# Optimization experiments

Measured on AMD Instinct MI355X. Metric: run time of the kernel, lower is better.

## Reference

```python
import jax, jax.numpy as jnp
import numpy as np

N = 100000          # nodes
E = 1600000         # edges
D_IN = 128
HID = 256
N_CLASSES = 10
N_GRAPHS = 64


def gcn_conv(x, src, dst, W, b, n_nodes):
    """PyG GCNConv: add self-loops, symmetric deg^{-1/2} normalization, x@W, scatter-add."""
    h = x @ W  # [N, out]
    loop = jnp.arange(n_nodes, dtype=src.dtype)
    src2 = jnp.concatenate([src, loop])
    dst2 = jnp.concatenate([dst, loop])
    deg = jax.ops.segment_sum(jnp.ones(src2.shape[0], x.dtype), dst2, num_segments=n_nodes)
    dinv = jax.lax.rsqrt(deg)  # deg >= 1 thanks to self-loops
    norm = dinv[src2] * dinv[dst2]  # [E+N]
    msg = norm[:, None] * h[src2]   # [E+N, out]
    return jax.ops.segment_sum(msg, dst2, num_segments=n_nodes) + b


def setup_inputs() -> dict:
    key = jax.random.key(0)
    ks = jax.random.split(key, 12)
    x = jax.random.normal(ks[0], (N, D_IN), dtype=jnp.float32)
    edge_index = jax.random.randint(ks[1], (2, E), 0, N, dtype=jnp.int64)
    batch = jnp.sort(jax.random.randint(ks[2], (N,), 0, N_GRAPHS, dtype=jnp.int64))
    def glorot(k, shape):
        lim = float(np.sqrt(6.0 / (shape[0] + shape[1])))
        return jax.random.uniform(k, shape, jnp.float32, -lim, lim)
    W1 = glorot(ks[3], (D_IN, HID));  b1 = jnp.zeros((HID,), jnp.float32)
    W2 = glorot(ks[4], (HID, HID));   b2 = jnp.zeros((HID,), jnp.float32)
    Wf1 = glorot(ks[5], (HID, HID));  bf1 = jnp.zeros((HID,), jnp.float32)
    Wf2 = glorot(ks[6], (HID, N_CLASSES)); bf2 = jnp.zeros((N_CLASSES,), jnp.float32)
    return {"x": x, "edge_index": edge_index, "batch": batch,
            "W1": W1, "b1": b1, "W2": W2, "b2": b2,
            "Wf1": Wf1, "bf1": bf1, "Wf2": Wf2, "bf2": bf2}


def reference(x, edge_index, batch, W1, b1, W2, b2, Wf1, bf1, Wf2, bf2):
    src, dst = edge_index[0], edge_index[1]
    h = jax.nn.relu(gcn_conv(x, src, dst, W1, b1, N))
    h = jax.nn.relu(gcn_conv(h, src, dst, W2, b2, N))
    # global mean pool over graph ids
    summed = jax.ops.segment_sum(h, batch, num_segments=N_GRAPHS)  # [G, HID]
    counts = jax.ops.segment_sum(jnp.ones((N,), h.dtype), batch, num_segments=N_GRAPHS)
    pooled = summed / jnp.maximum(counts, 1.0)[:, None]
    z = jax.nn.relu(pooled @ Wf1 + bf1)
    alpha = jax.nn.softplus(z @ Wf2 + bf2) + 0.001
    return alpha
```

## Files before the change

kernel.cpp:

```cpp
#include <hip/hip_runtime.h>
#include <math.h>

#define NN   100000
#define NE   1600000
#define DIN  128
#define HID  256
#define NG   64
#define NCLS 10

#define NBLK 128
#define EPB  (NE / NBLK)
#define NBUK 512
#define NPB  196
#define NHIST (NBUK * NBLK)
#define NBR  ((NN + 127) / 128)

using bf16x8 = __attribute__((ext_vector_type(8))) short;
using f32x4  = __attribute__((ext_vector_type(4))) float;
using f32x2  = __attribute__((ext_vector_type(2))) float;
using u32x2  = __attribute__((ext_vector_type(2))) unsigned int;
using u32x4  = __attribute__((ext_vector_type(4))) unsigned int;

static __device__ __forceinline__ unsigned short f2bf(float f) {
    unsigned u = __float_as_uint(f);
    u += 0x7fff + ((u >> 16) & 1);
    return (unsigned short)(u >> 16);
}

static __device__ __forceinline__ unsigned char f32_to_fp8(float f) {
    float a = fminf(fabsf(f), 448.f);
    unsigned bits = __float_as_uint(a * 0x1p-120f);
    bits += 0x7ffff + ((bits >> 20) & 1);
    unsigned e4 = (bits >> 20) & 0x7f;
    return (unsigned char)(e4 | (f < 0.f ? 0x80u : 0u));
}
#if __has_builtin(__builtin_amdgcn_cvt_pk_f32_fp8)
#define HAVE_CVT_FP8 1
#endif
static __device__ __forceinline__ void fp8x4_to_f32(unsigned u, float* f) {
#ifdef HAVE_CVT_FP8
    f32x2 lo = __builtin_amdgcn_cvt_pk_f32_fp8((int)u, false);
    f32x2 hi = __builtin_amdgcn_cvt_pk_f32_fp8((int)u, true);
    f[0] = lo[0]; f[1] = lo[1]; f[2] = hi[0]; f[3] = hi[1];
#else
#pragma unroll
    for (int k = 0; k < 4; ++k) {
        unsigned b = (u >> (8 * k)) & 0xffu;
        unsigned bits = ((b & 0x80u) << 24) | ((b & 0x7fu) << 20);
        f[k] = __uint_as_float(bits) * 0x1p+120f;
    }
#endif
}
static __device__ __forceinline__ int4 fp8x8_to_bf16x8(unsigned lo, unsigned hi) {
    float f[8];
    fp8x4_to_f32(lo, f);
    fp8x4_to_f32(hi, f + 4);
    int4 r;
    r.x = (int)((__float_as_uint(f[0]) >> 16) | (__float_as_uint(f[1]) & 0xffff0000u));
    r.y = (int)((__float_as_uint(f[2]) >> 16) | (__float_as_uint(f[3]) & 0xffff0000u));
    r.z = (int)((__float_as_uint(f[4]) >> 16) | (__float_as_uint(f[5]) & 0xffff0000u));
    r.w = (int)((__float_as_uint(f[6]) >> 16) | (__float_as_uint(f[7]) & 0xffff0000u));
    return r;
}


__global__ __launch_bounds__(256) void k_hist(const int* __restrict__ dst,
                                              int* __restrict__ histg) {
    __shared__ int h[NBUK];
    const int t = threadIdx.x;
    for (int i = t; i < NBUK; i += 256) h[i] = 0;
    __syncthreads();
    const int e0 = blockIdx.x * EPB, e1 = e0 + EPB;
    for (int e = e0 + t; e < e1; e += 256)
        atomicAdd(&h[(unsigned)__builtin_nontemporal_load(&dst[e]) / NPB], 1);
    __syncthreads();
    for (int i = t; i < NBUK; i += 256)
        histg[i * NBLK + blockIdx.x] = h[i];
}

__global__ __launch_bounds__(256) void k_bsum2(const int* __restrict__ d,
                                               int* __restrict__ bsum) {
    __shared__ int sd[256];
    int t = threadIdx.x;
    const int4 v = *(const int4*)&d[blockIdx.x * 1024 + t * 4];
    sd[t] = v.x + v.y + v.z + v.w;
    __syncthreads();
    for (int off = 128; off > 0; off >>= 1) {
        if (t < off) sd[t] += sd[t + off];
        __syncthreads();
    }
    if (t == 0) bsum[blockIdx.x] = sd[0];
}

__global__ void k_scanb2(const int* __restrict__ bsum, int* __restrict__ boff,
                         const int* __restrict__ batch, float* __restrict__ countsf) {
    __shared__ int tmp[64];
    int t = threadIdx.x;
    int v = bsum[t];
    tmp[t] = v; __syncthreads();
    for (int off = 1; off < 64; off <<= 1) {
        int u = (t >= off) ? tmp[t - off] : 0;
        __syncthreads();
        tmp[t] += u;
        __syncthreads();
    }
    boff[t] = tmp[t] - v;
    int g = t;
    int lo = 0, hi = NN;
    while (lo < hi) { int mid = (lo + hi) >> 1; if (batch[mid] < g) lo = mid + 1; else hi = mid; }
    int lb = lo;
    lo = 0; hi = NN;
    while (lo < hi) { int mid = (lo + hi) >> 1; if (batch[mid] <= g) lo = mid + 1; else hi = mid; }
    countsf[g] = (float)(lo - lb);
}

__global__ __launch_bounds__(256) void k_offs2(int* __restrict__ d,
                                               const int* __restrict__ boff) {
    __shared__ int ts[256];
    int t = threadIdx.x;
    int base = blockIdx.x * 1024 + t * 4;
    int4 v = *(const int4*)&d[base];
    int s = v.x + v.y + v.z + v.w;
    ts[t] = s; __syncthreads();
    for (int off = 1; off < 256; off <<= 1) {
        int u = (t >= off) ? ts[t - off] : 0;
        __syncthreads();
        ts[t] += u;
        __syncthreads();
    }
    int run = ts[t] - s + boff[blockIdx.x];
    int4 o;
    o.x = run; run += v.x;
    o.y = run; run += v.y;
    o.z = run; run += v.z;
    o.w = run; run += v.w;
    *(int4*)&d[base] = o;
}

__global__ __launch_bounds__(256) void k_scatter(const int* __restrict__ src,
                                                 const int* __restrict__ dst,
                                                 const int* __restrict__ offg,
                                                 unsigned* __restrict__ pairs) {
    __shared__ int cur[NBUK];
    const int t = threadIdx.x;
    for (int i = t; i < NBUK; i += 256) cur[i] = offg[i * NBLK + blockIdx.x];
    __syncthreads();
    const int e0 = blockIdx.x * EPB, e1 = e0 + EPB;
    for (int e = e0 + t; e < e1; e += 256) {
        int d = __builtin_nontemporal_load(&dst[e]);
        int sv = __builtin_nontemporal_load(&src[e]);
        int b = (unsigned)d / NPB;
        int li = d - b * NPB;
        unsigned pk = ((unsigned)li << 24) | (unsigned)sv;
        int p = atomicAdd(&cur[b], 1);
        __builtin_nontemporal_store(pk, &pairs[p]);
    }
}

__global__ __launch_bounds__(256) void k_csr(const unsigned* __restrict__ pairs,
                                             const int* __restrict__ offg,
                                             int* __restrict__ csr,
                                             int* __restrict__ deg,
                                             float* __restrict__ dinv,
                                             int* __restrict__ offs) {
    __shared__ int cnt[NPB];
    __shared__ int loff[256];
    __shared__ int cur[NPB];
    const int b = blockIdx.x, t = threadIdx.x;
    const int s     = offg[b * NBLK];
    const int e_end = (b == NBUK - 1) ? NE : offg[(b + 1) * NBLK];
    const int nb0   = b * NPB;
    const int nnod  = min(NPB, NN - nb0);
    if (t < NPB) cnt[t] = 0;
    __syncthreads();
    for (int e = s + t; e < e_end; e += 256)
        atomicAdd(&cnt[pairs[e] >> 24], 1);
    __syncthreads();
    int v = (t < NPB) ? cnt[t] : 0;
    loff[t] = v;
    __syncthreads();
    for (int off = 1; off < 256; off <<= 1) {
        int u = (t >= off) ? loff[t - off] : 0;
        __syncthreads();
        loff[t] += u;
        __syncthreads();
    }
    int myoff = loff[t] - v;
    __syncthreads();
    loff[t] = myoff;
    if (t < NPB) cur[t] = 0;
    __syncthreads();
    if (t < nnod) {
        int node = nb0 + t;
        int dg = cnt[t];
        deg[node]  = dg;
        dinv[node] = rsqrtf((float)(dg + 1));
        offs[node] = s + myoff;
    }
    for (int e = s + t; e < e_end; e += 256) {
        unsigned pk = pairs[e];
        int li = pk >> 24;
        int p = atomicAdd(&cur[li], 1);
        csr[s + loff[li] + p] = (int)(pk & 0xffffffu);
    }
}


#define XQ (NN * 32)

__global__ void k_cast_all(const float* __restrict__ x, const float* __restrict__ dinv,
                           unsigned char* __restrict__ xs8,
                           const float* __restrict__ W1, unsigned short* __restrict__ Wt1,
                           const float* __restrict__ W2, unsigned short* __restrict__ Wt2) {
    int i = blockIdx.x * blockDim.x + threadIdx.x;
    if (i < XQ) {
        int nd = i >> 5;
        int q  = i & 31;
        float dv = dinv[nd];
        const float4 v = *(const float4*)&x[(size_t)nd * DIN + q * 4];
        uchar4 o;
        o.x = f32_to_fp8(v.x * dv); o.y = f32_to_fp8(v.y * dv);
        o.z = f32_to_fp8(v.z * dv); o.w = f32_to_fp8(v.w * dv);
        *(uchar4*)&xs8[(size_t)nd * DIN + q * 4] = o;
        return;
    }
    int j = i - XQ;
    if (j < DIN * HID) {
        int k = j >> 8, nc = j & 255;
        Wt1[nc * DIN + k] = f2bf(W1[j]);
    } else if (j < (DIN + HID) * HID) {
        int jj = j - DIN * HID;
        int k = jj >> 8, nc = jj & 255;
        Wt2[nc * HID + k] = f2bf(W2[jj]);
    }
}


template <int MODE>
__global__ __launch_bounds__(512) void k_gemm_mfma(const unsigned char* __restrict__ A8,
                                                   const unsigned short* __restrict__ Wt,
                                                   const float* __restrict__ dinv,
                                                   const float* __restrict__ bias,
                                                   void* __restrict__ outp,
                                                   const int* __restrict__ batch,
                                                   int M, int K) {
    __shared__ unsigned short As[128 * 72];
    __shared__ unsigned short Bs[256 * 72];
    __shared__ float psum[4][256];
    __shared__ int gloc[128];
    const int t = threadIdx.x;
    const int lane = t & 63;
    const int wid = t >> 6;
    const int wr = wid & 1, wc = wid >> 1;
    const int bm = blockIdx.x * 128;
    const int lr = lane & 15;
    const int ko = (lane >> 4) << 3;

    f32x4 acc[4][4] = {};

    const int arow = t >> 2;
    const int akq  = (t & 3) << 4;
    const int brow = t >> 1;
    const int bkq  = (t & 1) << 5;

    int g0 = 0, gend = 0;
    if (MODE == 2) {
        g0 = batch[bm];
        gend = batch[min(bm + 127, M - 1)];
        for (int i = t; i < 4 * 256; i += 512) ((float*)psum)[i] = 0.f;
        if (t < 128) gloc[t] = (bm + t < M) ? min(batch[bm + t] - g0, 3) : 0;
    }

    for (int kk = 0; kk < K; kk += 64) {
        {
            int row = bm + arow;
            u32x4 v; v.x = v.y = v.z = v.w = 0u;
            if (row < M) v = *(const u32x4*)&A8[(size_t)row * K + kk + akq];
            *(int4*)&As[arow * 72 + akq]     = fp8x8_to_bf16x8(v.x, v.y);
            *(int4*)&As[arow * 72 + akq + 8] = fp8x8_to_bf16x8(v.z, v.w);
        }
        {
            const unsigned short* wsrc = &Wt[(size_t)brow * K + kk + bkq];
#pragma unroll
            for (int q = 0; q < 4; ++q)
                *(int4*)&Bs[brow * 72 + bkq + q * 8] = *(const int4*)&wsrc[q * 8];
        }
        __syncthreads();
#pragma unroll
        for (int ks = 0; ks < 64; ks += 32) {
            bf16x8 af[4], bfr[4];
#pragma unroll
            for (int mf = 0; mf < 4; ++mf)
                af[mf] = *(const bf16x8*)&As[(wr * 64 + mf * 16 + lr) * 72 + ks + ko];
#pragma unroll
            for (int nf = 0; nf < 4; ++nf)
                bfr[nf] = *(const bf16x8*)&Bs[(wc * 64 + nf * 16 + lr) * 72 + ks + ko];
#pragma unroll
            for (int mf = 0; mf < 4; ++mf)
#pragma unroll
                for (int nf = 0; nf < 4; ++nf)
                    acc[mf][nf] = __builtin_amdgcn_mfma_f32_16x16x32_bf16(af[mf], bfr[nf], acc[mf][nf], 0, 0, 0);
        }
        __syncthreads();
    }

    if (MODE == 1) {
        unsigned char* out8 = (unsigned char*)outp;
#pragma unroll
        for (int mf = 0; mf < 4; ++mf) {
#pragma unroll
            for (int b = 0; b < 4; ++b) {
                int row = bm + wr * 64 + mf * 16 + (lane >> 4) * 4 + b;
                if (row >= M) continue;
                float dv = dinv[row];
#pragma unroll
                for (int nf = 0; nf < 4; ++nf) {
                    int col = wc * 64 + nf * 16 + lr;
                    float v = fmaxf(acc[mf][nf][b] + bias[col], 0.f);
                    out8[(size_t)row * HID + col] = f32_to_fp8(dv * v);
                }
            }
        }
    } else {
        const int q4 = (lane >> 4) << 2;
        if (gend == g0) {
#pragma unroll
            for (int nf = 0; nf < 4; ++nf) {
                const int lcol = wc * 64 + nf * 16 + lr;
                const float bb = bias[lcol];
                float rsum = 0.f;
#pragma unroll
                for (int mf = 0; mf < 4; ++mf)
#pragma unroll
                    for (int b = 0; b < 4; ++b) {
                        int lrow = wr * 64 + mf * 16 + q4 + b;
                        if (bm + lrow < M) rsum += fmaxf(acc[mf][nf][b] + bb, 0.f);
                    }
                rsum += __shfl_xor(rsum, 16);
                rsum += __shfl_xor(rsum, 32);
                if ((lane >> 4) == 0) atomicAdd(&psum[0][lcol], rsum);
            }
        } else {
#pragma unroll
            for (int nf = 0; nf < 4; ++nf) {
                const int lcol = wc * 64 + nf * 16 + lr;
                const float bb = bias[lcol];
                float run = 0.f; int gcur = 0;
#pragma unroll
                for (int mf = 0; mf < 4; ++mf) {
#pragma unroll
                    for (int b = 0; b < 4; ++b) {
                        int lrow = wr * 64 + mf * 16 + q4 + b;
                        if (bm + lrow < M) {
                            int gl = gloc[lrow];
                            float v = fmaxf(acc[mf][nf][b] + bb, 0.f);
                            if (gl != gcur) {
                                if (run != 0.f) atomicAdd(&psum[gcur][lcol], run);
                                run = 0.f; gcur = gl;
                            }
                            run += v;
                        }
                    }
                }
                if (run != 0.f) atomicAdd(&psum[gcur][lcol], run);
            }
        }
        __syncthreads();
        float* scratch = (float*)outp;
        size_t base = (size_t)blockIdx.x * 1024;
        for (int i = t; i < 1024; i += 512)
            __builtin_nontemporal_store(((const float*)psum)[i], &scratch[base + i]);
    }
}


__global__ __launch_bounds__(256) void k_agg256(const unsigned char* __restrict__ hs,
                                                const int* __restrict__ csr,
                                                const int* __restrict__ offs,
                                                const int* __restrict__ deg,
                                                const float* __restrict__ dinv,
                                                unsigned char* __restrict__ out, int n) {
    int wid = threadIdx.x >> 6, lane = threadIdx.x & 63;
    int node = blockIdx.x * 4 + wid;
    if (node >= n) return;
    int c = lane << 2;
    float a0, a1, a2, a3;
    {
        unsigned u = *(const unsigned*)&hs[(size_t)node * HID + c];
        float f[4]; fp8x4_to_f32(u, f);
        a0 = f[0]; a1 = f[1]; a2 = f[2]; a3 = f[3];
    }
    int s0 = offs[node], cnt = deg[node];
    for (int base = 0; base < cnt; base += 64) {
        int nb = min(64, cnt - base);
        int idx = (lane < nb) ? __builtin_nontemporal_load(&csr[s0 + base + lane]) : 0;
        int i = 0;
        for (; i + 8 <= nb; i += 8) {
            unsigned v[8];
#pragma unroll
            for (int k = 0; k < 8; ++k) {
                int j = __shfl(idx, i + k);
                v[k] = *(const unsigned*)&hs[(size_t)j * HID + c];
            }
#pragma unroll
            for (int k = 0; k < 8; ++k) {
                float f[4]; fp8x4_to_f32(v[k], f);
                a0 += f[0]; a1 += f[1]; a2 += f[2]; a3 += f[3];
            }
        }
        for (; i + 4 <= nb; i += 4) {
            unsigned v[4];
#pragma unroll
            for (int k = 0; k < 4; ++k) {
                int j = __shfl(idx, i + k);
                v[k] = *(const unsigned*)&hs[(size_t)j * HID + c];
            }
#pragma unroll
            for (int k = 0; k < 4; ++k) {
                float f[4]; fp8x4_to_f32(v[k], f);
                a0 += f[0]; a1 += f[1]; a2 += f[2]; a3 += f[3];
            }
        }
        for (; i < nb; ++i) {
            int j = __shfl(idx, i);
            unsigned u = *(const unsigned*)&hs[(size_t)j * HID + c];
            float f[4]; fp8x4_to_f32(u, f);
            a0 += f[0]; a1 += f[1]; a2 += f[2]; a3 += f[3];
        }
    }
    float dv = dinv[node];
    uchar4 r;
    r.x = f32_to_fp8(dv * a0); r.y = f32_to_fp8(dv * a1);
    r.z = f32_to_fp8(dv * a2); r.w = f32_to_fp8(dv * a3);
    *(uchar4*)&out[(size_t)node * HID + c] = r;
}


__global__ __launch_bounds__(256) void k_agg128(const unsigned char* __restrict__ xs,
                                                const int* __restrict__ csr,
                                                const int* __restrict__ offs,
                                                const int* __restrict__ deg,
                                                const float* __restrict__ dinv,
                                                unsigned char* __restrict__ out, int n) {
    int wid = threadIdx.x >> 6, lane = threadIdx.x & 63;
    int node = blockIdx.x * 4 + wid;
    if (node >= n) return;
    int half = lane >> 5, l32 = lane & 31;
    int c = l32 << 2;
    float a0 = 0.f, a1 = 0.f, a2 = 0.f, a3 = 0.f;
    if (half == 0) {
        unsigned u = *(const unsigned*)&xs[(size_t)node * DIN + c];
        float f[4]; fp8x4_to_f32(u, f);
        a0 = f[0]; a1 = f[1]; a2 = f[2]; a3 = f[3];
    }
    int s0 = offs[node], cnt = deg[node];
    for (int base = 0; base < cnt; base += 64) {
        int nb = min(64, cnt - base);
        int idx = (lane < nb) ? __builtin_nontemporal_load(&csr[s0 + base + lane]) : 0;
        int i = 0;
        for (; i + 8 <= nb; i += 8) {
            unsigned v[4];
#pragma unroll
            for (int k = 0; k < 4; ++k) {
                int j = __shfl(idx, i + 2 * k + half);
                v[k] = *(const unsigned*)&xs[(size_t)j * DIN + c];
            }
#pragma unroll
            for (int k = 0; k < 4; ++k) {
                float f[4]; fp8x4_to_f32(v[k], f);
                a0 += f[0]; a1 += f[1]; a2 += f[2]; a3 += f[3];
            }
        }
        for (; i < nb; i += 2) {
            int e = i + half;
            int j = __shfl(idx, e < nb ? e : 0);
            if (e < nb) {
                unsigned u = *(const unsigned*)&xs[(size_t)j * DIN + c];
                float f[4]; fp8x4_to_f32(u, f);
                a0 += f[0]; a1 += f[1]; a2 += f[2]; a3 += f[3];
            }
        }
    }
    a0 += __shfl_xor(a0, 32);
    a1 += __shfl_xor(a1, 32);
    a2 += __shfl_xor(a2, 32);
    a3 += __shfl_xor(a3, 32);
    if (half == 0) {
        float dv = dinv[node];
        uchar4 r;
        r.x = f32_to_fp8(dv * a0); r.y = f32_to_fp8(dv * a1);
        r.z = f32_to_fp8(dv * a2); r.w = f32_to_fp8(dv * a3);
        *(uchar4*)&out[(size_t)node * DIN + c] = r;
    }
}


__global__ __launch_bounds__(256) void k_mlp(const float* __restrict__ scratch,
                                             const int* __restrict__ batch,
                                             const float* __restrict__ countsf,
                                             const float* __restrict__ Wf1,
                                             const float* __restrict__ bf1,
                                             const float* __restrict__ Wf2,
                                             const float* __restrict__ bf2,
                                             float* __restrict__ out) {
    __shared__ float p[HID];
    __shared__ float z[HID];
    int g = blockIdx.x, t = threadIdx.x;
    int lo = 0, hi = NN;
    while (lo < hi) { int mid = (lo + hi) >> 1; if (batch[mid] < g) lo = mid + 1; else hi = mid; }
    int s = lo;
    lo = s; hi = NN;
    while (lo < hi) { int mid = (lo + hi) >> 1; if (batch[mid] <= g) lo = mid + 1; else hi = mid; }
    int e = lo;
    float sum = 0.f;
    if (e > s) {
        int bx0 = s >> 7, bx1 = (e - 1) >> 7;
        for (int bx = bx0; bx <= bx1; ++bx) {
            int gl = min(g - batch[bx << 7], 3);
            sum += scratch[(size_t)bx * 1024 + gl * 256 + t];
        }
    }
    float cnt = fmaxf(countsf[g], 1.0f);
    p[t] = sum / cnt;
    __syncthreads();
    float accz = bf1[t];
    for (int k = 0; k < HID; ++k)
        accz = fmaf(p[k], Wf1[k * HID + t], accz);
    z[t] = fmaxf(accz, 0.f);
    __syncthreads();
    if (t < NCLS) {
        float o = bf2[t];
        for (int k = 0; k < HID; ++k)
            o = fmaf(z[k], Wf2[k * NCLS + t], o);
        float sp = fmaxf(o, 0.f) + log1pf(expf(-fabsf(o)));
        out[g * NCLS + t] = sp + 0.001f;
    }
}


extern "C" void kernel_launch(void* const* d_in, const int* in_sizes, int n_in,
                              void* d_out, int out_size, void* d_ws, size_t ws_size,
                              hipStream_t stream) {
    const float* x     = (const float*)d_in[0];
    const int*   ei    = (const int*)d_in[1];
    const int*   batch = (const int*)d_in[2];
    const float* W1    = (const float*)d_in[3];
    const float* b1    = (const float*)d_in[4];
    const float* W2    = (const float*)d_in[5];
    const float* b2    = (const float*)d_in[6];
    const float* Wf1   = (const float*)d_in[7];
    const float* bf1   = (const float*)d_in[8];
    const float* Wf2   = (const float*)d_in[9];
    const float* bf2   = (const float*)d_in[10];
    float* out = (float*)d_out;

    const int* srcv = ei;
    const int* dstv = ei + NE;

    char* p = (char*)d_ws;
    auto take = [&](size_t bytes) -> char* {
        char* q = p; p += (bytes + 255) & ~(size_t)255; return q;
    };
    char* big0 = take((size_t)NN * HID * 2);
    char* big1 = take((size_t)NN * HID * 2);
    unsigned char*  xs8 = (unsigned char*)big0;
    unsigned char*  xa8 = (unsigned char*)(big0 + (size_t)NN * DIN);
    unsigned char*  h8  = (unsigned char*)big1;
    unsigned char*  r8  = (unsigned char*)big0;
    float* scratch = (float*)(big1 + (size_t)NN * HID);
    unsigned* pairs = (unsigned*)big1;
    unsigned short* wt1  = (unsigned short*)take((size_t)DIN * HID * 2);
    unsigned short* wt2  = (unsigned short*)take((size_t)HID * HID * 2);
    int*   histg   = (int*)take((size_t)NHIST * 4);
    int*   bsum    = (int*)take(64 * 4);
    int*   boff    = (int*)take(64 * 4);
    int*   deg     = (int*)take((size_t)NN * 4);
    int*   offs    = (int*)take((size_t)NN * 4);
    int*   csr     = (int*)take((size_t)NE * 4);
    float* dinv    = (float*)take((size_t)NN * 4);
    float* countsf = (float*)take((size_t)NG * 4);

    k_hist<<<NBLK, 256, 0, stream>>>(dstv, histg);
    k_bsum2<<<64, 256, 0, stream>>>(histg, bsum);
    k_scanb2<<<1, 64, 0, stream>>>(bsum, boff, batch, countsf);
    k_offs2<<<64, 256, 0, stream>>>(histg, boff);
    k_scatter<<<NBLK, 256, 0, stream>>>(srcv, dstv, histg, pairs);
    k_csr<<<NBUK, 256, 0, stream>>>(pairs, histg, csr, deg, dinv, offs);

    int cast_total = XQ + (DIN + HID) * HID;
    k_cast_all<<<(cast_total + 255) / 256, 256, 0, stream>>>(x, dinv, xs8, W1, wt1, W2, wt2);

    k_agg128<<<(NN + 3) / 4, 256, 0, stream>>>(xs8, csr, offs, deg, dinv, xa8, NN);
    k_gemm_mfma<1><<<NBR, 512, 0, stream>>>(xa8, wt1, dinv, b1, (void*)h8, batch, NN, DIN);
    k_agg256<<<(NN + 3) / 4, 256, 0, stream>>>(h8, csr, offs, deg, dinv, r8, NN);
    k_gemm_mfma<2><<<NBR, 512, 0, stream>>>(r8, wt2, dinv, b2, (void*)scratch, batch, NN, HID);

    k_mlp<<<NG, 256, 0, stream>>>(scratch, batch, countsf, Wf1, bf1, Wf2, bf2, out);
}
```

Baseline: 324.4 us.

## Fuse input/weight casts into histogram kernel and apply dinv in aggregation

The standalone cast kernel is merged into the histogram launch as extra blocks, which requires removing its dependence on dinv (not yet computed at that point). To compensate, the first aggregation kernel now loads dinv[j] per neighbor and multiplies it in via FMA, and scales the self term by dinv[node]. This removes one kernel launch and lets the casting overlap with histogram work. In exchange the aggregation does an extra scattered 4-byte gather per edge, and fp8 quantization now happens before the dinv scaling, which slightly changes numerics.

Result: faster. 310.4 us, median of 4 (-4.3%).

```diff
diff --git a/kernel.cpp b/kernel.cpp
--- a/kernel.cpp
+++ b/kernel.cpp
@@ -14,6 +14,10 @@
 #define NPB  196
 #define NHIST (NBUK * NBLK)
 #define NBR  ((NN + 127) / 128)
+
+#define XQ (NN * 32)
+#define CAST_TOTAL (XQ + (DIN + HID) * HID)
+#define CAST_BLKS  ((CAST_TOTAL + 255) / 256)
 
 using bf16x8 = __attribute__((ext_vector_type(8))) short;
 using f32x4  = __attribute__((ext_vector_type(4))) float;
@@ -65,9 +69,38 @@
 
 
 __global__ __launch_bounds__(256) void k_hist(const int* __restrict__ dst,
-                                              int* __restrict__ histg) {
+                                              int* __restrict__ histg,
+                                              const float* __restrict__ x,
+                                              unsigned char* __restrict__ xs8,
+                                              const float* __restrict__ W1,
+                                              unsigned short* __restrict__ Wt1,
+                                              const float* __restrict__ W2,
+                                              unsigned short* __restrict__ Wt2) {
+    const int t = threadIdx.x;
+    if (blockIdx.x >= NBLK) {
+        int i = (blockIdx.x - NBLK) * 256 + t;
+        if (i < XQ) {
+            int nd = i >> 5;
+            int q  = i & 31;
+            const float4 v = *(const float4*)&x[(size_t)nd * DIN + q * 4];
+            uchar4 o;
+            o.x = f32_to_fp8(v.x); o.y = f32_to_fp8(v.y);
+            o.z = f32_to_fp8(v.z); o.w = f32_to_fp8(v.w);
+            *(uchar4*)&xs8[(size_t)nd * DIN + q * 4] = o;
+        } else {
+            int j = i - XQ;
+            if (j < DIN * HID) {
+                int k = j >> 8, nc = j & 255;
+                Wt1[nc * DIN + k] = f2bf(W1[j]);
+            } else if (j < (DIN + HID) * HID) {
+                int jj = j - DIN * HID;
+                int k = jj >> 8, nc = jj & 255;
+                Wt2[nc * HID + k] = f2bf(W2[jj]);
+            }
+        }
+        return;
+    }
     __shared__ int h[NBUK];
-    const int t = threadIdx.x;
     for (int i = t; i < NBUK; i += 256) h[i] = 0;
     __syncthreads();
     const int e0 = blockIdx.x * EPB, e1 = e0 + EPB;
@@ -202,36 +235,6 @@
         int li = pk >> 24;
         int p = atomicAdd(&cur[li], 1);
         csr[s + loff[li] + p] = (int)(pk & 0xffffffu);
-    }
-}
-
-
-#define XQ (NN * 32)
-
-__global__ void k_cast_all(const float* __restrict__ x, const float* __restrict__ dinv,
-                           unsigned char* __restrict__ xs8,
-                           const float* __restrict__ W1, unsigned short* __restrict__ Wt1,
-                           const float* __restrict__ W2, unsigned short* __restrict__ Wt2) {
-    int i = blockIdx.x * blockDim.x + threadIdx.x;
-    if (i < XQ) {
-        int nd = i >> 5;
-        int q  = i & 31;
-        float dv = dinv[nd];
-        const float4 v = *(const float4*)&x[(size_t)nd * DIN + q * 4];
-        uchar4 o;
-        o.x = f32_to_fp8(v.x * dv); o.y = f32_to_fp8(v.y * dv);
-        o.z = f32_to_fp8(v.z * dv); o.w = f32_to_fp8(v.w * dv);
-        *(uchar4*)&xs8[(size_t)nd * DIN + q * 4] = o;
-        return;
-    }
-    int j = i - XQ;
-    if (j < DIN * HID) {
-        int k = j >> 8, nc = j & 255;
-        Wt1[nc * DIN + k] = f2bf(W1[j]);
-    } else if (j < (DIN + HID) * HID) {
-        int jj = j - DIN * HID;
-        int k = jj >> 8, nc = jj & 255;
-        Wt2[nc * HID + k] = f2bf(W2[jj]);
     }
 }
 
@@ -447,11 +450,12 @@
     if (node >= n) return;
     int half = lane >> 5, l32 = lane & 31;
     int c = l32 << 2;
+    float dvn = dinv[node];
     float a0 = 0.f, a1 = 0.f, a2 = 0.f, a3 = 0.f;
     if (half == 0) {
         unsigned u = *(const unsigned*)&xs[(size_t)node * DIN + c];
         float f[4]; fp8x4_to_f32(u, f);
-        a0 = f[0]; a1 = f[1]; a2 = f[2]; a3 = f[3];
+        a0 = dvn * f[0]; a1 = dvn * f[1]; a2 = dvn * f[2]; a3 = dvn * f[3];
     }
     int s0 = offs[node], cnt = deg[node];
     for (int base = 0; base < cnt; base += 64) {
@@ -459,16 +463,18 @@
         int idx = (lane < nb) ? __builtin_nontemporal_load(&csr[s0 + base + lane]) : 0;
         int i = 0;
         for (; i + 8 <= nb; i += 8) {
-            unsigned v[4];
+            unsigned v[4]; float dvj[4];
 #pragma unroll
             for (int k = 0; k < 4; ++k) {
                 int j = __shfl(idx, i + 2 * k + half);
                 v[k] = *(const unsigned*)&xs[(size_t)j * DIN + c];
+                dvj[k] = dinv[j];
             }
 #pragma unroll
             for (int k = 0; k < 4; ++k) {
                 float f[4]; fp8x4_to_f32(v[k], f);
-                a0 += f[0]; a1 += f[1]; a2 += f[2]; a3 += f[3];
+                a0 = fmaf(dvj[k], f[0], a0); a1 = fmaf(dvj[k], f[1], a1);
+                a2 = fmaf(dvj[k], f[2], a2); a3 = fmaf(dvj[k], f[3], a3);
             }
         }
         for (; i < nb; i += 2) {
@@ -476,8 +482,10 @@
             int j = __shfl(idx, e < nb ? e : 0);
             if (e < nb) {
                 unsigned u = *(const unsigned*)&xs[(size_t)j * DIN + c];
+                float dvj = dinv[j];
                 float f[4]; fp8x4_to_f32(u, f);
-                a0 += f[0]; a1 += f[1]; a2 += f[2]; a3 += f[3];
+                a0 = fmaf(dvj, f[0], a0); a1 = fmaf(dvj, f[1], a1);
+                a2 = fmaf(dvj, f[2], a2); a3 = fmaf(dvj, f[3], a3);
             }
         }
     }
@@ -486,10 +494,9 @@
     a2 += __shfl_xor(a2, 32);
     a3 += __shfl_xor(a3, 32);
     if (half == 0) {
-        float dv = dinv[node];
         uchar4 r;
-        r.x = f32_to_fp8(dv * a0); r.y = f32_to_fp8(dv * a1);
-        r.z = f32_to_fp8(dv * a2); r.w = f32_to_fp8(dv * a3);
+        r.x = f32_to_fp8(dvn * a0); r.y = f32_to_fp8(dvn * a1);
+        r.z = f32_to_fp8(dvn * a2); r.w = f32_to_fp8(dvn * a3);
         *(uchar4*)&out[(size_t)node * DIN + c] = r;
     }
 }
@@ -580,16 +587,13 @@
     float* dinv    = (float*)take((size_t)NN * 4);
     float* countsf = (float*)take((size_t)NG * 4);
 
-    k_hist<<<NBLK, 256, 0, stream>>>(dstv, histg);
+    k_hist<<<NBLK + CAST_BLKS, 256, 0, stream>>>(dstv, histg, x, xs8, W1, wt1, W2, wt2);
     k_bsum2<<<64, 256, 0, stream>>>(histg, bsum);
     k_scanb2<<<1, 64, 0, stream>>>(bsum, boff, batch, countsf);
     k_offs2<<<64, 256, 0, stream>>>(histg, boff);
     k_scatter<<<NBLK, 256, 0, stream>>>(srcv, dstv, histg, pairs);
     k_csr<<<NBUK, 256, 0, stream>>>(pairs, histg, csr, deg, dinv, offs);
 
-    int cast_total = XQ + (DIN + HID) * HID;
-    k_cast_all<<<(cast_total + 255) / 256, 256, 0, stream>>>(x, dinv, xs8, W1, wt1, W2, wt2);
-
     k_agg128<<<(NN + 3) / 4, 256, 0, stream>>>(xs8, csr, offs, deg, dinv, xa8, NN);
     k_gemm_mfma<1><<<NBR, 512, 0, stream>>>(xa8, wt1, dinv, b1, (void*)h8, batch, NN, DIN);
     k_agg256<<<(NN + 3) / 4, 256, 0, stream>>>(h8, csr, offs, deg, dinv, r8, NN);
```
